# Performance work log

Hardware: AMD Instinct MI355X
Metric: run time of the kernel (lower is better)

Reference implementation:

```python
import jax, jax.numpy as jnp
import numpy as np

EPS_LN = 1e-5
ALPHA_THRESH = 1.0 / 255.0


def _make_coord(X, Y):
    # make_coord((X,Y), flatten=True): centers in [-1,1], row-major over (X,Y)
    cx = (jnp.arange(X, dtype=jnp.float32) + 0.5) / X * 2.0 - 1.0
    cy = (jnp.arange(Y, dtype=jnp.float32) + 0.5) / Y * 2.0 - 1.0
    gx, gy = jnp.meshgrid(cx, cy, indexing='ij')
    return jnp.stack([gx.reshape(-1), gy.reshape(-1)], axis=-1)  # [X*Y, 2]


def _mlp(x, w1, b1, w2, b2):
    return jax.nn.relu(x @ w1 + b1) @ w2 + b2


def _unfold3x3(feat):
    # feat: [B,C,X,Y] -> torch F.unfold(3, padding=1) layout [B, C*9, X, Y]
    B, C, X, Y = feat.shape
    fp = jnp.pad(feat, ((0, 0), (0, 0), (1, 1), (1, 1)))
    patches = jnp.stack([fp[:, :, ki:ki + X, kj:kj + Y]
                         for ki in range(3) for kj in range(3)], axis=2)  # [B,C,9,X,Y]
    return patches.reshape(B, C * 9, X, Y)


def _render_one(xy, scale, rot, color, H, W):
    # project_gaussians_2d_scale_rot: ndc -> pixel centers
    cx = 0.5 * ((xy[:, 0] + 1.0) * W - 1.0)  # [N]
    cy = 0.5 * ((xy[:, 1] + 1.0) * H - 1.0)
    c, s = jnp.cos(rot[:, 0]), jnp.sin(rot[:, 0])
    sx2, sy2 = scale[:, 0] ** 2, scale[:, 1] ** 2
    cov00 = c * c * sx2 + s * s * sy2
    cov01 = c * s * (sx2 - sy2)
    cov11 = s * s * sx2 + c * c * sy2
    det = cov00 * cov11 - cov01 * cov01
    A = cov11 / det   # conic xx
    Bc = -cov01 / det  # conic xy
    Cc = cov00 / det  # conic yy
    px = jnp.arange(W, dtype=jnp.float32)
    py = jnp.arange(H, dtype=jnp.float32)
    dx = px[None, :, None] - cx[None, None, :]  # [1,W,N] -> broadcast [H,W,N]
    dy = py[:, None, None] - cy[None, None, :]  # [H,1,N]
    sigma = 0.5 * (A * dx * dx + Cc * dy * dy) + Bc * dx * dy  # [H,W,N]
    alpha = jnp.exp(-sigma)  # opacity = 1
    alpha = jnp.where(alpha >= ALPHA_THRESH, alpha, 0.0)  # rasterizer skip threshold
    img = jnp.einsum('hwn,nc->hwc', alpha, color)  # sum-compositing
    img = jnp.clip(img, 0.0, 1.0)
    return jnp.transpose(img, (2, 0, 1))  # [3,H,W]


def reference(inp, conv_w, conv_b,
              off_w1, off_b1, off_w2, off_b2,
              sc_w1, sc_b1, sc_w2, sc_b2,
              rot_w1, rot_b1, rot_w2, rot_b2,
              col_w1, col_b1, col_w2, col_b2,
              target_h, target_w):
    H0, W0 = inp.shape[-2], inp.shape[-1]
    factor = max(target_h / H0, target_w / W0)
    # encoder: 3x3 conv, same padding
    feat = jax.lax.conv_general_dilated(
        inp, conv_w, (1, 1), 'SAME',
        dimension_numbers=('NCHW', 'OIHW', 'NCHW')) + conv_b[None, :, None, None]
    feat = jnp.transpose(feat, (0, 1, 3, 2))  # [B,C,X=W0,Y=H0]
    B, C, X, Y = feat.shape
    feat = _unfold3x3(feat)  # [B,C*9,X,Y]
    feat = jnp.transpose(feat, (0, 2, 3, 1)).reshape(B, X * Y, C * 9)
    mu = jnp.mean(feat, axis=-1, keepdims=True)
    var = jnp.var(feat, axis=-1, keepdims=True)
    feat = (feat - mu) / jnp.sqrt(var + EPS_LN)
    coord = _make_coord(X, Y)[None]  # [1,N,2]
    off_factor = 2.0 * factor / max(target_h, target_w)
    offset = jnp.tanh(_mlp(feat, off_w1, off_b1, off_w2, off_b2)) * 3.0 * off_factor
    xy = coord + offset                                               # [B,N,2]
    scale = jax.nn.sigmoid(_mlp(feat, sc_w1, sc_b1, sc_w2, sc_b2)) * 2.0 * factor
    rot = jax.nn.sigmoid(_mlp(feat, rot_w1, rot_b1, rot_w2, rot_b2)) * 2.0 * jnp.pi
    color = jnp.tanh(_mlp(feat, col_w1, col_b1, col_w2, col_b2))
    render = jax.vmap(lambda a, b, c2, d: _render_one(a, b, c2, d, target_h, target_w))
    return render(xy, scale, rot, color)  # [B,3,H,W]


def setup_inputs() -> dict:
    key = jax.random.key(0)
    ks = jax.random.split(key, 16)
    d_in, hid = 288, 256

    def lin(k, fan_in, shape):
        return jax.random.normal(k, shape, jnp.float32) / np.sqrt(fan_in)

    return {
        'inp': jax.random.uniform(ks[0], (1, 3, 48, 48), jnp.float32),
        'conv_w': lin(ks[1], 27, (32, 3, 3, 3)),
        'conv_b': jnp.zeros((32,), jnp.float32),
        'off_w1': lin(ks[2], d_in, (d_in, hid)), 'off_b1': jnp.zeros((hid,), jnp.float32),
        'off_w2': lin(ks[3], hid, (hid, 2)), 'off_b2': jnp.zeros((2,), jnp.float32),
        'sc_w1': lin(ks[4], d_in, (d_in, hid)), 'sc_b1': jnp.zeros((hid,), jnp.float32),
        'sc_w2': lin(ks[5], hid, (hid, 2)), 'sc_b2': jnp.zeros((2,), jnp.float32),
        'rot_w1': lin(ks[6], d_in, (d_in, hid)), 'rot_b1': jnp.zeros((hid,), jnp.float32),
        'rot_w2': lin(ks[7], hid, (hid, 1)), 'rot_b2': jnp.zeros((1,), jnp.float32),
        'col_w1': lin(ks[8], d_in, (d_in, hid)), 'col_b1': jnp.zeros((hid,), jnp.float32),
        'col_w2': lin(ks[9], hid, (hid, 3)), 'col_b2': jnp.zeros((3,), jnp.float32),
        'target_h': 192,
        'target_w': 192,
    }
```

## Files before the change

### kernel.cpp

```cpp
#include <hip/hip_runtime.h>

#define NXY   48
#define NG    2304
#define CFE   32
#define KDIM  288
#define HID   256
#define NHID  1024
#define HW    192
#define NPIX  (HW*HW)
#define NCHUNK (NG/64)

typedef __bf16 bf16x8 __attribute__((ext_vector_type(8)));
typedef float  f32x4  __attribute__((ext_vector_type(4)));
typedef unsigned short ushort_t;
typedef unsigned int   uint_t;

__device__ __forceinline__ ushort_t f2bf(float x) {
    uint_t u = __float_as_uint(x);
    uint_t r = u + 0x7FFFu + ((u >> 16) & 1u);
    return (ushort_t)(r >> 16);
}
__device__ __forceinline__ float bf2f(ushort_t h) {
    return __uint_as_float(((uint_t)h) << 16);
}

__global__ __launch_bounds__(256) void conv_k(const float* __restrict__ inp,
                                              const float* __restrict__ cw,
                                              const float* __restrict__ cb,
                                              float* __restrict__ feat) {
    int idx = blockIdx.x * 256 + threadIdx.x;
    if (idx >= CFE * NXY * NXY) return;
    int w = idx % NXY, h = (idx / NXY) % NXY, o = idx / (NXY * NXY);
    float acc = cb[o];
    #pragma unroll
    for (int i = 0; i < 3; ++i) {
        #pragma unroll
        for (int kh = 0; kh < 3; ++kh) {
            int hh = h + kh - 1;
            if (hh < 0 || hh >= NXY) continue;
            #pragma unroll
            for (int kw = 0; kw < 3; ++kw) {
                int ww = w + kw - 1;
                if (ww < 0 || ww >= NXY) continue;
                acc = fmaf(inp[(i * NXY + hh) * NXY + ww],
                           cw[((o * 3 + i) * 3 + kh) * 3 + kw], acc);
            }
        }
    }
    feat[idx] = acc;
}

__global__ __launch_bounds__(64) void ln_k(const float* __restrict__ feat,
                                           ushort_t* __restrict__ Ahi,
                                           ushort_t* __restrict__ Alo) {
    int n = blockIdx.x;
    int lane = threadIdx.x;
    int x = n / NXY, y = n % NXY;
    float v[5];
    float sum = 0.f, sq = 0.f;
    #pragma unroll
    for (int i = 0; i < 5; ++i) {
        int k = lane + 64 * i;
        float val = 0.f;
        if (k < KDIM) {
            int c = k / 9, r = k % 9, ki = r / 3, kj = r % 3;
            int hh = y + kj - 1, ww = x + ki - 1;
            if (hh >= 0 && hh < NXY && ww >= 0 && ww < NXY)
                val = feat[(c * NXY + hh) * NXY + ww];
        }
        v[i] = val; sum += val; sq = fmaf(val, val, sq);
    }
    #pragma unroll
    for (int off = 32; off; off >>= 1) {
        sum += __shfl_xor(sum, off);
        sq  += __shfl_xor(sq,  off);
    }
    float mean = sum * (1.0f / KDIM);
    float var  = sq * (1.0f / KDIM) - mean * mean;
    float rstd = rsqrtf(var + 1e-5f);
    #pragma unroll
    for (int i = 0; i < 5; ++i) {
        int k = lane + 64 * i;
        if (k < KDIM) {
            float w = (v[i] - mean) * rstd;
            ushort_t hb = f2bf(w);
            ushort_t lb = f2bf(w - bf2f(hb));
            Ahi[n * KDIM + k] = hb;
            Alo[n * KDIM + k] = lb;
        }
    }
}

__global__ __launch_bounds__(256) void w1pack_k(const float* __restrict__ w0,
        const float* __restrict__ w1, const float* __restrict__ w2,
        const float* __restrict__ w3,
        ushort_t* __restrict__ Bph, ushort_t* __restrict__ Bpl) {
    int tid = blockIdx.x * 256 + threadIdx.x;
    if (tid >= 64 * 9 * 64) return;
    int l = tid & 63;
    int t = tid >> 6;
    int ks = t % 9, nf = t / 9;
    int ncol = nf * 16 + (l & 15);
    int head = ncol >> 8, c = ncol & 255;
    const float* w = head == 0 ? w0 : head == 1 ? w1 : head == 2 ? w2 : w3;
    int kbase = ks * 32 + (l >> 4) * 8;
    ushort_t hb[8], lb[8];
    #pragma unroll
    for (int i = 0; i < 8; ++i) {
        float x = w[(kbase + i) * HID + c];
        hb[i] = f2bf(x);
        lb[i] = f2bf(x - bf2f(hb[i]));
    }
    #pragma unroll
    for (int i = 0; i < 8; ++i) {
        Bph[tid * 8 + i] = hb[i];
        Bpl[tid * 8 + i] = lb[i];
    }
}

__global__ __launch_bounds__(128) void gemm_k(const ushort_t* __restrict__ Ahi,
        const ushort_t* __restrict__ Alo,
        const ushort_t* __restrict__ Bph, const ushort_t* __restrict__ Bpl,
        const float* __restrict__ b1_0, const float* __restrict__ b1_1,
        const float* __restrict__ b1_2, const float* __restrict__ b1_3,
        float* __restrict__ Hout) {
    int l  = threadIdx.x & 63;
    int wv = threadIdx.x >> 6;
    int m0 = blockIdx.x * 128 + wv * 64;
    int n0 = blockIdx.y * 64;
    int r15 = l & 15, kg = l >> 4;
    f32x4 acc[4][4] = {};
    const ushort_t* pah = Ahi + (m0 + r15) * KDIM + kg * 8;
    const ushort_t* pal = Alo + (m0 + r15) * KDIM + kg * 8;
    for (int ks = 0; ks < 9; ++ks) {
        bf16x8 ah[4], al[4], bh[4], bl[4];
        #pragma unroll
        for (int m = 0; m < 4; ++m) {
            ah[m] = *(const bf16x8*)(pah + m * 16 * KDIM + ks * 32);
            al[m] = *(const bf16x8*)(pal + m * 16 * KDIM + ks * 32);
        }
        #pragma unroll
        for (int n = 0; n < 4; ++n) {
            size_t off = ((size_t)((blockIdx.y * 4 + n) * 9 + ks) * 64 + l) * 8;
            bh[n] = *(const bf16x8*)(Bph + off);
            bl[n] = *(const bf16x8*)(Bpl + off);
        }
        #pragma unroll
        for (int m = 0; m < 4; ++m)
            #pragma unroll
            for (int n = 0; n < 4; ++n) {
                acc[m][n] = __builtin_amdgcn_mfma_f32_16x16x32_bf16(ah[m], bh[n], acc[m][n], 0, 0, 0);
                acc[m][n] = __builtin_amdgcn_mfma_f32_16x16x32_bf16(ah[m], bl[n], acc[m][n], 0, 0, 0);
                acc[m][n] = __builtin_amdgcn_mfma_f32_16x16x32_bf16(al[m], bh[n], acc[m][n], 0, 0, 0);
            }
    }
    #pragma unroll
    for (int n = 0; n < 4; ++n) {
        int col = n0 + n * 16 + r15;
        int head = col >> 8;
        const float* bb = head == 0 ? b1_0 : head == 1 ? b1_1 : head == 2 ? b1_2 : b1_3;
        float bias = bb[col & 255];
        #pragma unroll
        for (int m = 0; m < 4; ++m)
            #pragma unroll
            for (int r = 0; r < 4; ++r) {
                int grow = m0 + m * 16 + kg * 4 + r;
                Hout[grow * NHID + col] = fmaxf(acc[m][n][r] + bias, 0.f);
            }
    }
}

__global__ __launch_bounds__(256) void head_k(const float* __restrict__ Hh,
        const float* __restrict__ ow2, const float* __restrict__ ob2,
        const float* __restrict__ sw2, const float* __restrict__ sb2,
        const float* __restrict__ rw2, const float* __restrict__ rb2,
        const float* __restrict__ cw2, const float* __restrict__ cb2,
        float4* __restrict__ gbox, float4* __restrict__ gdat) {
    int tid = threadIdx.x;
    int lane = tid & 63, wv = tid >> 6;
    int n = blockIdx.x * 4 + wv;
    const float* h = Hh + n * NHID;
    float s[8] = {};
    #pragma unroll
    for (int i = 0; i < 4; ++i) {
        int j = lane + 64 * i;
        float h0 = h[j], h1 = h[256 + j], h2 = h[512 + j], h3 = h[768 + j];
        s[0] = fmaf(h0, ow2[j * 2 + 0], s[0]);
        s[1] = fmaf(h0, ow2[j * 2 + 1], s[1]);
        s[2] = fmaf(h1, sw2[j * 2 + 0], s[2]);
        s[3] = fmaf(h1, sw2[j * 2 + 1], s[3]);
        s[4] = fmaf(h2, rw2[j],         s[4]);
        s[5] = fmaf(h3, cw2[j * 3 + 0], s[5]);
        s[6] = fmaf(h3, cw2[j * 3 + 1], s[6]);
        s[7] = fmaf(h3, cw2[j * 3 + 2], s[7]);
    }
    #pragma unroll
    for (int off = 32; off; off >>= 1)
        #pragma unroll
        for (int k = 0; k < 8; ++k) s[k] += __shfl_xor(s[k], off);
    if (lane == 0) {
        float o0 = s[0] + ob2[0], o1 = s[1] + ob2[1];
        float z0 = s[2] + sb2[0], z1 = s[3] + sb2[1];
        float zr = s[4] + rb2[0];
        float c0 = s[5] + cb2[0], c1 = s[6] + cb2[1], c2 = s[7] + cb2[2];
        int x = n / NXY, y = n % NXY;
        float ndcx = ((x + 0.5f) * (2.0f / NXY) - 1.0f) + tanhf(o0) * 0.125f;
        float ndcy = ((y + 0.5f) * (2.0f / NXY) - 1.0f) + tanhf(o1) * 0.125f;
        float cxp = 0.5f * ((ndcx + 1.0f) * HW - 1.0f);
        float cyp = 0.5f * ((ndcy + 1.0f) * HW - 1.0f);
        float sx = 8.0f / (1.0f + expf(-z0));
        float sy = 8.0f / (1.0f + expf(-z1));
        float rot = 6.283185307179586f / (1.0f + expf(-zr));
        float cc = cosf(rot), ss = sinf(rot);
        float sx2 = sx * sx, sy2 = sy * sy;
        float cov00 = cc * cc * sx2 + ss * ss * sy2;
        float cov01 = cc * ss * (sx2 - sy2);
        float cov11 = ss * ss * sx2 + cc * cc * sy2;
        float det = cov00 * cov11 - cov01 * cov01;
        float inv = 1.0f / det;
        float A = cov11 * inv, Bc = -cov01 * inv, Cc = cov00 * inv;
        float rx = sqrtf(11.2f * cov00) + 1e-2f;
        float ry = sqrtf(11.2f * cov11) + 1e-2f;
        gbox[n]         = make_float4(cxp, cyp, rx, ry);
        gdat[2 * n]     = make_float4(0.5f * A, Bc, 0.5f * Cc, tanhf(c0));
        gdat[2 * n + 1] = make_float4(tanhf(c1), tanhf(c2), 0.f, 0.f);
    }
}

__global__ __launch_bounds__(256) void render_k(const float4* __restrict__ gbox,
                                                const float4* __restrict__ gdat,
                                                float* __restrict__ out) {
    __shared__ float4 ldsE[4][64][2];
    __shared__ float red[4][64][3];
    int lane = threadIdx.x & 63;
    int wv   = threadIdx.x >> 6;
    int tx0 = blockIdx.x * 8, ty0 = blockIdx.y * 8;
    float px = (float)(tx0 + (lane & 7));
    float py = (float)(ty0 + (lane >> 3));
    float xlo = (float)tx0, xhi = (float)(tx0 + 7);
    float ylo = (float)ty0, yhi = (float)(ty0 + 7);
    float ar = 0.f, ag = 0.f, ab = 0.f;
    for (int c = wv; c < NCHUNK; c += 4) {
        int g = c * 64 + lane;
        float4 bb = gbox[g];
        bool pred = (bb.x - bb.z <= xhi) && (bb.x + bb.z >= xlo) &&
                    (bb.y - bb.w <= yhi) && (bb.y + bb.w >= ylo);
        unsigned long long m = __ballot(pred);
        int cnt = __popcll(m);
        int pos = __popcll(m & ((1ull << lane) - 1ull));
        if (pred) {
            float4 d0 = gdat[2 * g];
            float4 d1 = gdat[2 * g + 1];
            ldsE[wv][pos][0] = make_float4(bb.x, bb.y, d0.x, d0.y);
            ldsE[wv][pos][1] = make_float4(d0.z, d0.w, d1.x, d1.y);
        }
        __syncthreads();
        for (int i = 0; i < cnt; ++i) {
            float4 e0 = ldsE[wv][i][0];
            float4 e1 = ldsE[wv][i][1];
            float dx = px - e0.x;
            float dy = py - e0.y;
            float sigma = fmaf(dx, fmaf(e0.z, dx, e0.w * dy), e1.x * dy * dy);
            float a = __expf(-sigma);
            a = (a >= (1.0f / 255.0f)) ? a : 0.f;
            ar = fmaf(a, e1.y, ar);
            ag = fmaf(a, e1.z, ag);
            ab = fmaf(a, e1.w, ab);
        }
        __syncthreads();
    }
    red[wv][lane][0] = ar; red[wv][lane][1] = ag; red[wv][lane][2] = ab;
    __syncthreads();
    if (wv == 0) {
        float r_ = red[0][lane][0] + red[1][lane][0] + red[2][lane][0] + red[3][lane][0];
        float g_ = red[0][lane][1] + red[1][lane][1] + red[2][lane][1] + red[3][lane][1];
        float b_ = red[0][lane][2] + red[1][lane][2] + red[2][lane][2] + red[3][lane][2];
        int pix = (ty0 + (lane >> 3)) * HW + tx0 + (lane & 7);
        out[pix]            = fminf(fmaxf(r_, 0.f), 1.f);
        out[NPIX + pix]     = fminf(fmaxf(g_, 0.f), 1.f);
        out[2 * NPIX + pix] = fminf(fmaxf(b_, 0.f), 1.f);
    }
}

extern "C" void kernel_launch(void* const* d_in, const int* in_sizes, int n_in,
                              void* d_out, int out_size, void* d_ws, size_t ws_size,
                              hipStream_t stream) {
    const float* inp = (const float*)d_in[0];
    const float* cw  = (const float*)d_in[1];
    const float* cb  = (const float*)d_in[2];
    const float* ow1 = (const float*)d_in[3];
    const float* ob1 = (const float*)d_in[4];
    const float* ow2 = (const float*)d_in[5];
    const float* ob2 = (const float*)d_in[6];
    const float* sw1 = (const float*)d_in[7];
    const float* sb1 = (const float*)d_in[8];
    const float* sw2 = (const float*)d_in[9];
    const float* sb2 = (const float*)d_in[10];
    const float* rw1 = (const float*)d_in[11];
    const float* rb1 = (const float*)d_in[12];
    const float* rw2 = (const float*)d_in[13];
    const float* rb2 = (const float*)d_in[14];
    const float* cw1 = (const float*)d_in[15];
    const float* cb1 = (const float*)d_in[16];
    const float* cw2 = (const float*)d_in[17];
    const float* cb2 = (const float*)d_in[18];

    float* ws = (float*)d_ws;
    float*    feat = ws;
    float*    hid  = ws + 73728;
    float4*   gbox = (float4*)(ws + 2433024);
    float4*   gdat = (float4*)(ws + 2442240);
    ushort_t* Ahi  = (ushort_t*)(ws + 2460672);
    ushort_t* Alo  = (ushort_t*)(ws + 2792448);
    ushort_t* Bph  = (ushort_t*)(ws + 3124224);
    ushort_t* Bpl  = (ushort_t*)(ws + 3271680);
    float* out = (float*)d_out;

    hipLaunchKernelGGL(conv_k, dim3(288), dim3(256), 0, stream, inp, cw, cb, feat);
    hipLaunchKernelGGL(ln_k, dim3(NG), dim3(64), 0, stream, feat, Ahi, Alo);
    hipLaunchKernelGGL(w1pack_k, dim3(144), dim3(256), 0, stream,
                       ow1, sw1, rw1, cw1, Bph, Bpl);
    hipLaunchKernelGGL(gemm_k, dim3(18, 16), dim3(128), 0, stream,
                       Ahi, Alo, Bph, Bpl, ob1, sb1, rb1, cb1, hid);
    hipLaunchKernelGGL(head_k, dim3(576), dim3(256), 0, stream,
                       hid, ow2, ob2, sw2, sb2, rw2, rb2, cw2, cb2, gbox, gdat);
    hipLaunchKernelGGL(render_k, dim3(24, 24), dim3(256), 0, stream, gbox, gdat, out);
}
```

Before: 53.19 us.

## Fuse conv+LN+weight pack into one kernel and GEMM with head MLP

Conv, layernorm and weight packing now run in a single prep kernel: the conv output is recomputed inline per unfolded element instead of being written to a feature buffer, and weight packing uses extra blocks of the same launch. The first-layer GEMM is fused with the second-layer head reduction, so hidden activations stay in LDS instead of round-tripping through global memory. The render loop also swaps block-wide barriers for a wave-local LDS wait, since each wave only reads its own staging slot. The cost is redundant conv arithmetic (9x recomputation) and a GEMM with a smaller per-wave tile, which gives less register-level reuse.

```diff
diff --git a/kernel.cpp b/kernel.cpp
--- a/kernel.cpp
+++ b/kernel.cpp
@@ -2,7 +2,6 @@
 
 #define NXY   48
 #define NG    2304
-#define CFE   32
 #define KDIM  288
 #define HID   256
 #define NHID  1024
@@ -24,166 +23,132 @@
     return __uint_as_float(((uint_t)h) << 16);
 }
 
-__global__ __launch_bounds__(256) void conv_k(const float* __restrict__ inp,
-                                              const float* __restrict__ cw,
-                                              const float* __restrict__ cb,
-                                              float* __restrict__ feat) {
-    int idx = blockIdx.x * 256 + threadIdx.x;
-    if (idx >= CFE * NXY * NXY) return;
-    int w = idx % NXY, h = (idx / NXY) % NXY, o = idx / (NXY * NXY);
-    float acc = cb[o];
-    #pragma unroll
-    for (int i = 0; i < 3; ++i) {
-        #pragma unroll
-        for (int kh = 0; kh < 3; ++kh) {
-            int hh = h + kh - 1;
-            if (hh < 0 || hh >= NXY) continue;
-            #pragma unroll
-            for (int kw = 0; kw < 3; ++kw) {
-                int ww = w + kw - 1;
-                if (ww < 0 || ww >= NXY) continue;
-                acc = fmaf(inp[(i * NXY + hh) * NXY + ww],
-                           cw[((o * 3 + i) * 3 + kh) * 3 + kw], acc);
+__global__ __launch_bounds__(256) void prep_k(const float* __restrict__ inp,
+        const float* __restrict__ cw, const float* __restrict__ cb,
+        const float* __restrict__ pw0, const float* __restrict__ pw1,
+        const float* __restrict__ pw2, const float* __restrict__ pw3,
+        ushort_t* __restrict__ Ahi, ushort_t* __restrict__ Alo,
+        ushort_t* __restrict__ Bph, ushort_t* __restrict__ Bpl) {
+    int bx = blockIdx.x;
+    if (bx < 576) {
+        int lane = threadIdx.x & 63;
+        int n = bx * 4 + (threadIdx.x >> 6);
+        int x = n / NXY, y = n % NXY;
+        float v[5];
+        float sum = 0.f, sq = 0.f;
+        #pragma unroll
+        for (int i = 0; i < 5; ++i) {
+            int k = lane + 64 * i;
+            float val = 0.f;
+            if (k < KDIM) {
+                int c = k / 9, r = k % 9, ki = r / 3, kj = r % 3;
+                int hh = y + kj - 1, ww = x + ki - 1;
+                if (hh >= 0 && hh < NXY && ww >= 0 && ww < NXY) {
+                    val = cb[c];
+                    #pragma unroll
+                    for (int i3 = 0; i3 < 3; ++i3)
+                        #pragma unroll
+                        for (int kh = 0; kh < 3; ++kh) {
+                            int h2 = hh + kh - 1;
+                            if (h2 < 0 || h2 >= NXY) continue;
+                            #pragma unroll
+                            for (int kw = 0; kw < 3; ++kw) {
+                                int w2 = ww + kw - 1;
+                                if (w2 < 0 || w2 >= NXY) continue;
+                                val = fmaf(inp[(i3 * NXY + h2) * NXY + w2],
+                                           cw[((c * 3 + i3) * 3 + kh) * 3 + kw], val);
+                            }
+                        }
+                }
             }
-        }
-    }
-    feat[idx] = acc;
-}
-
-__global__ __launch_bounds__(64) void ln_k(const float* __restrict__ feat,
-                                           ushort_t* __restrict__ Ahi,
-                                           ushort_t* __restrict__ Alo) {
-    int n = blockIdx.x;
-    int lane = threadIdx.x;
-    int x = n / NXY, y = n % NXY;
-    float v[5];
-    float sum = 0.f, sq = 0.f;
-    #pragma unroll
-    for (int i = 0; i < 5; ++i) {
-        int k = lane + 64 * i;
-        float val = 0.f;
-        if (k < KDIM) {
-            int c = k / 9, r = k % 9, ki = r / 3, kj = r % 3;
-            int hh = y + kj - 1, ww = x + ki - 1;
-            if (hh >= 0 && hh < NXY && ww >= 0 && ww < NXY)
-                val = feat[(c * NXY + hh) * NXY + ww];
-        }
-        v[i] = val; sum += val; sq = fmaf(val, val, sq);
-    }
-    #pragma unroll
-    for (int off = 32; off; off >>= 1) {
-        sum += __shfl_xor(sum, off);
-        sq  += __shfl_xor(sq,  off);
-    }
-    float mean = sum * (1.0f / KDIM);
-    float var  = sq * (1.0f / KDIM) - mean * mean;
-    float rstd = rsqrtf(var + 1e-5f);
-    #pragma unroll
-    for (int i = 0; i < 5; ++i) {
-        int k = lane + 64 * i;
-        if (k < KDIM) {
-            float w = (v[i] - mean) * rstd;
-            ushort_t hb = f2bf(w);
-            ushort_t lb = f2bf(w - bf2f(hb));
-            Ahi[n * KDIM + k] = hb;
-            Alo[n * KDIM + k] = lb;
-        }
-    }
-}
-
-__global__ __launch_bounds__(256) void w1pack_k(const float* __restrict__ w0,
-        const float* __restrict__ w1, const float* __restrict__ w2,
-        const float* __restrict__ w3,
-        ushort_t* __restrict__ Bph, ushort_t* __restrict__ Bpl) {
-    int tid = blockIdx.x * 256 + threadIdx.x;
-    if (tid >= 64 * 9 * 64) return;
-    int l = tid & 63;
-    int t = tid >> 6;
-    int ks = t % 9, nf = t / 9;
-    int ncol = nf * 16 + (l & 15);
-    int head = ncol >> 8, c = ncol & 255;
-    const float* w = head == 0 ? w0 : head == 1 ? w1 : head == 2 ? w2 : w3;
-    int kbase = ks * 32 + (l >> 4) * 8;
-    ushort_t hb[8], lb[8];
-    #pragma unroll
-    for (int i = 0; i < 8; ++i) {
-        float x = w[(kbase + i) * HID + c];
-        hb[i] = f2bf(x);
-        lb[i] = f2bf(x - bf2f(hb[i]));
-    }
-    #pragma unroll
-    for (int i = 0; i < 8; ++i) {
-        Bph[tid * 8 + i] = hb[i];
-        Bpl[tid * 8 + i] = lb[i];
-    }
-}
-
-__global__ __launch_bounds__(128) void gemm_k(const ushort_t* __restrict__ Ahi,
-        const ushort_t* __restrict__ Alo,
+            v[i] = val; sum += val; sq = fmaf(val, val, sq);
+        }
+        #pragma unroll
+        for (int off = 32; off; off >>= 1) {
+            sum += __shfl_xor(sum, off);
+            sq  += __shfl_xor(sq,  off);
+        }
+        float mean = sum * (1.0f / KDIM);
+        float var  = sq * (1.0f / KDIM) - mean * mean;
+        float rstd = rsqrtf(var + 1e-5f);
+        #pragma unroll
+        for (int i = 0; i < 5; ++i) {
+            int k = lane + 64 * i;
+            if (k < KDIM) {
+                float w = (v[i] - mean) * rstd;
+                ushort_t hb = f2bf(w);
+                ushort_t lb = f2bf(w - bf2f(hb));
+                Ahi[n * KDIM + k] = hb;
+                Alo[n * KDIM + k] = lb;
+            }
+        }
+    } else {
+        int tid = (bx - 576) * 256 + threadIdx.x;
+        int l = tid & 63;
+        int t = tid >> 6;
+        int ks = t % 9, nf = t / 9;
+        int ncol = nf * 16 + (l & 15);
+        int head = ncol >> 8, c = ncol & 255;
+        const float* w = head == 0 ? pw0 : head == 1 ? pw1 : head == 2 ? pw2 : pw3;
+        int kbase = ks * 32 + (l >> 4) * 8;
+        #pragma unroll
+        for (int i = 0; i < 8; ++i) {
+            float x = w[(kbase + i) * HID + c];
+            ushort_t hb = f2bf(x);
+            Bph[tid * 8 + i] = hb;
+            Bpl[tid * 8 + i] = f2bf(x - bf2f(hb));
+        }
+    }
+}
+
+__global__ __launch_bounds__(1024) void gemmhead_k(
+        const ushort_t* __restrict__ Ahi, const ushort_t* __restrict__ Alo,
         const ushort_t* __restrict__ Bph, const ushort_t* __restrict__ Bpl,
-        const float* __restrict__ b1_0, const float* __restrict__ b1_1,
-        const float* __restrict__ b1_2, const float* __restrict__ b1_3,
-        float* __restrict__ Hout) {
-    int l  = threadIdx.x & 63;
-    int wv = threadIdx.x >> 6;
-    int m0 = blockIdx.x * 128 + wv * 64;
-    int n0 = blockIdx.y * 64;
-    int r15 = l & 15, kg = l >> 4;
-    f32x4 acc[4][4] = {};
-    const ushort_t* pah = Ahi + (m0 + r15) * KDIM + kg * 8;
-    const ushort_t* pal = Alo + (m0 + r15) * KDIM + kg * 8;
-    for (int ks = 0; ks < 9; ++ks) {
-        bf16x8 ah[4], al[4], bh[4], bl[4];
-        #pragma unroll
-        for (int m = 0; m < 4; ++m) {
-            ah[m] = *(const bf16x8*)(pah + m * 16 * KDIM + ks * 32);
-            al[m] = *(const bf16x8*)(pal + m * 16 * KDIM + ks * 32);
-        }
-        #pragma unroll
-        for (int n = 0; n < 4; ++n) {
-            size_t off = ((size_t)((blockIdx.y * 4 + n) * 9 + ks) * 64 + l) * 8;
-            bh[n] = *(const bf16x8*)(Bph + off);
-            bl[n] = *(const bf16x8*)(Bpl + off);
-        }
-        #pragma unroll
-        for (int m = 0; m < 4; ++m)
-            #pragma unroll
-            for (int n = 0; n < 4; ++n) {
-                acc[m][n] = __builtin_amdgcn_mfma_f32_16x16x32_bf16(ah[m], bh[n], acc[m][n], 0, 0, 0);
-                acc[m][n] = __builtin_amdgcn_mfma_f32_16x16x32_bf16(ah[m], bl[n], acc[m][n], 0, 0, 0);
-                acc[m][n] = __builtin_amdgcn_mfma_f32_16x16x32_bf16(al[m], bh[n], acc[m][n], 0, 0, 0);
-            }
-    }
-    #pragma unroll
-    for (int n = 0; n < 4; ++n) {
-        int col = n0 + n * 16 + r15;
-        int head = col >> 8;
-        const float* bb = head == 0 ? b1_0 : head == 1 ? b1_1 : head == 2 ? b1_2 : b1_3;
-        float bias = bb[col & 255];
-        #pragma unroll
-        for (int m = 0; m < 4; ++m)
-            #pragma unroll
-            for (int r = 0; r < 4; ++r) {
-                int grow = m0 + m * 16 + kg * 4 + r;
-                Hout[grow * NHID + col] = fmaxf(acc[m][n][r] + bias, 0.f);
-            }
-    }
-}
-
-__global__ __launch_bounds__(256) void head_k(const float* __restrict__ Hh,
+        const float* __restrict__ ob1, const float* __restrict__ sb1,
+        const float* __restrict__ rb1, const float* __restrict__ cb1,
         const float* __restrict__ ow2, const float* __restrict__ ob2,
         const float* __restrict__ sw2, const float* __restrict__ sb2,
         const float* __restrict__ rw2, const float* __restrict__ rb2,
         const float* __restrict__ cw2, const float* __restrict__ cb2,
         float4* __restrict__ gbox, float4* __restrict__ gdat) {
-    int tid = threadIdx.x;
-    int lane = tid & 63, wv = tid >> 6;
-    int n = blockIdx.x * 4 + wv;
-    const float* h = Hh + n * NHID;
+    __shared__ float ldsH[16][1028];
+    int l  = threadIdx.x & 63;
+    int w  = threadIdx.x >> 6;
+    int g0 = blockIdx.x * 16;
+    int r15 = l & 15, kg = l >> 4;
+    f32x4 acc[4] = {};
+    const ushort_t* pah = Ahi + (g0 + r15) * KDIM + kg * 8;
+    const ushort_t* pal = Alo + (g0 + r15) * KDIM + kg * 8;
+    #pragma unroll
+    for (int ks = 0; ks < 9; ++ks) {
+        bf16x8 ah = *(const bf16x8*)(pah + ks * 32);
+        bf16x8 al = *(const bf16x8*)(pal + ks * 32);
+        #pragma unroll
+        for (int n = 0; n < 4; ++n) {
+            size_t off = ((size_t)((w * 4 + n) * 9 + ks) * 64 + l) * 8;
+            bf16x8 bh = *(const bf16x8*)(Bph + off);
+            bf16x8 bl = *(const bf16x8*)(Bpl + off);
+            acc[n] = __builtin_amdgcn_mfma_f32_16x16x32_bf16(ah, bh, acc[n], 0, 0, 0);
+            acc[n] = __builtin_amdgcn_mfma_f32_16x16x32_bf16(ah, bl, acc[n], 0, 0, 0);
+            acc[n] = __builtin_amdgcn_mfma_f32_16x16x32_bf16(al, bh, acc[n], 0, 0, 0);
+        }
+    }
+    int hd = w >> 2;
+    const float* bb = hd == 0 ? ob1 : hd == 1 ? sb1 : hd == 2 ? rb1 : cb1;
+    #pragma unroll
+    for (int n = 0; n < 4; ++n) {
+        int col = w * 64 + n * 16 + r15;
+        float bias = bb[col & 255];
+        #pragma unroll
+        for (int r = 0; r < 4; ++r)
+            ldsH[kg * 4 + r][col] = fmaxf(acc[n][r] + bias, 0.f);
+    }
+    __syncthreads();
+    const float* h = ldsH[w];
     float s[8] = {};
     #pragma unroll
     for (int i = 0; i < 4; ++i) {
-        int j = lane + 64 * i;
+        int j = l + 64 * i;
         float h0 = h[j], h1 = h[256 + j], h2 = h[512 + j], h3 = h[768 + j];
         s[0] = fmaf(h0, ow2[j * 2 + 0], s[0]);
         s[1] = fmaf(h0, ow2[j * 2 + 1], s[1]);
@@ -198,7 +163,8 @@
     for (int off = 32; off; off >>= 1)
         #pragma unroll
         for (int k = 0; k < 8; ++k) s[k] += __shfl_xor(s[k], off);
-    if (lane == 0) {
+    if (l == 0) {
+        int n = g0 + w;
         float o0 = s[0] + ob2[0], o1 = s[1] + ob2[1];
         float z0 = s[2] + sb2[0], z1 = s[3] + sb2[1];
         float zr = s[4] + rb2[0];
@@ -254,7 +220,7 @@
             ldsE[wv][pos][0] = make_float4(bb.x, bb.y, d0.x, d0.y);
             ldsE[wv][pos][1] = make_float4(d0.z, d0.w, d1.x, d1.y);
         }
-        __syncthreads();
+        asm volatile("s_waitcnt lgkmcnt(0)" ::: "memory");
         for (int i = 0; i < cnt; ++i) {
             float4 e0 = ldsE[wv][i][0];
             float4 e1 = ldsE[wv][i][1];
@@ -267,7 +233,6 @@
             ag = fmaf(a, e1.z, ag);
             ab = fmaf(a, e1.w, ab);
         }
-        __syncthreads();
     }
     red[wv][lane][0] = ar; red[wv][lane][1] = ag; red[wv][lane][2] = ab;
     __syncthreads();
@@ -306,23 +271,18 @@
     const float* cb2 = (const float*)d_in[18];
 
     float* ws = (float*)d_ws;
-    float*    feat = ws;
-    float*    hid  = ws + 73728;
-    float4*   gbox = (float4*)(ws + 2433024);
-    float4*   gdat = (float4*)(ws + 2442240);
-    ushort_t* Ahi  = (ushort_t*)(ws + 2460672);
-    ushort_t* Alo  = (ushort_t*)(ws + 2792448);
-    ushort_t* Bph  = (ushort_t*)(ws + 3124224);
-    ushort_t* Bpl  = (ushort_t*)(ws + 3271680);
+    ushort_t* Ahi  = (ushort_t*)ws;
+    ushort_t* Alo  = (ushort_t*)(ws + 331776);
+    ushort_t* Bph  = (ushort_t*)(ws + 663552);
+    ushort_t* Bpl  = (ushort_t*)(ws + 811008);
+    float4*   gbox = (float4*)(ws + 958464);
+    float4*   gdat = (float4*)(ws + 967680);
     float* out = (float*)d_out;
 
-    hipLaunchKernelGGL(conv_k, dim3(288), dim3(256), 0, stream, inp, cw, cb, feat);
-    hipLaunchKernelGGL(ln_k, dim3(NG), dim3(64), 0, stream, feat, Ahi, Alo);
-    hipLaunchKernelGGL(w1pack_k, dim3(144), dim3(256), 0, stream,
-                       ow1, sw1, rw1, cw1, Bph, Bpl);
-    hipLaunchKernelGGL(gemm_k, dim3(18, 16), dim3(128), 0, stream,
-                       Ahi, Alo, Bph, Bpl, ob1, sb1, rb1, cb1, hid);
-    hipLaunchKernelGGL(head_k, dim3(576), dim3(256), 0, stream,
-                       hid, ow2, ob2, sw2, sb2, rw2, rb2, cw2, cb2, gbox, gdat);
+    hipLaunchKernelGGL(prep_k, dim3(720), dim3(256), 0, stream,
+                       inp, cw, cb, ow1, sw1, rw1, cw1, Ahi, Alo, Bph, Bpl);
+    hipLaunchKernelGGL(gemmhead_k, dim3(144), dim3(1024), 0, stream,
+                       Ahi, Alo, Bph, Bpl, ob1, sb1, rb1, cb1,
+                       ow2, ob2, sw2, sb2, rw2, rb2, cw2, cb2, gbox, gdat);
     hipLaunchKernelGGL(render_k, dim3(24, 24), dim3(256), 0, stream, gbox, gdat, out);
 }
```

New measurement: 60.88 us. +14.5%, slower.
